# Kernel optimization log

Measured on AMD Instinct MI355X. Metric: run time of the kernel, lower is better.

## Reference

```python
import jax, jax.numpy as jnp
import numpy as np

DIM = 128
NUM_TILES = 50000
NUM_PIECES = 25000
E_TT = 600000
E_PT = 400000


def _mean_aggregate(msgs, dst, num_dst):
    # msgs: [E, dim], dst: [E] int -> [num_dst, dim]
    agg = jax.ops.segment_sum(msgs, dst, num_segments=num_dst)
    cnt = jax.ops.segment_sum(jnp.ones((dst.shape[0], 1), msgs.dtype), dst,
                              num_segments=num_dst)
    return agg / jnp.maximum(cnt, 1.0)


def _linear(x, W, b):
    # torch nn.Linear: y = x @ W.T + b, W: [out, in]
    return x @ W.T + b


def setup_inputs() -> dict:
    key = jax.random.key(0)
    ks = jax.random.split(key, 20)
    s = 1.0 / np.sqrt(DIM)
    s2 = 1.0 / np.sqrt(2 * DIM)
    inp = {
        "tile_h": jax.random.normal(ks[0], (NUM_TILES, DIM), jnp.float32),
        "piece_h": jax.random.normal(ks[1], (NUM_PIECES, DIM), jnp.float32),
        "tile_src": jax.random.randint(ks[2], (E_PT,), 0, NUM_TILES),
        "piece_dst": jax.random.randint(ks[3], (E_PT,), 0, NUM_PIECES),
        "piece_src": jax.random.randint(ks[4], (E_PT,), 0, NUM_PIECES),
        "tile_dst": jax.random.randint(ks[5], (E_PT,), 0, NUM_TILES),
        "t_src": jax.random.randint(ks[6], (E_TT,), 0, NUM_TILES),
        "t_dst": jax.random.randint(ks[7], (E_TT,), 0, NUM_TILES),
        # weights: torch Linear layout [out_features, in_features]
        "W_t2p": jax.random.uniform(ks[8], (DIM, DIM), jnp.float32, -s, s),
        "b_t2p": jax.random.uniform(ks[9], (DIM,), jnp.float32, -s, s),
        "W_pu": jax.random.uniform(ks[10], (DIM, 2 * DIM), jnp.float32, -s2, s2),
        "b_pu": jax.random.uniform(ks[11], (DIM,), jnp.float32, -s2, s2),
        "W_p2t": jax.random.uniform(ks[12], (DIM, DIM), jnp.float32, -s, s),
        "b_p2t": jax.random.uniform(ks[13], (DIM,), jnp.float32, -s, s),
        "W_tup": jax.random.uniform(ks[14], (DIM, 2 * DIM), jnp.float32, -s2, s2),
        "b_tup": jax.random.uniform(ks[15], (DIM,), jnp.float32, -s2, s2),
        "W_t2t": jax.random.uniform(ks[16], (DIM, DIM), jnp.float32, -s, s),
        "b_t2t": jax.random.uniform(ks[17], (DIM,), jnp.float32, -s, s),
        "W_tut": jax.random.uniform(ks[18], (DIM, 2 * DIM), jnp.float32, -s2, s2),
        "b_tut": jax.random.uniform(ks[19], (DIM,), jnp.float32, -s2, s2),
    }
    return inp


def reference(tile_h, piece_h, tile_src, piece_dst, piece_src, tile_dst,
              t_src, t_dst,
              W_t2p, b_t2p, W_pu, b_pu, W_p2t, b_p2t,
              W_tup, b_tup, W_t2t, b_t2t, W_tut, b_tut):
    num_tiles = tile_h.shape[0]
    num_pieces = piece_h.shape[0]

    # Stage 1: tile -> piece
    msgs = _linear(tile_h[tile_src], W_t2p, b_t2p)          # [E_pt, dim]
    agg = _mean_aggregate(msgs, piece_dst, num_pieces)
    piece_h = jax.nn.relu(_linear(jnp.concatenate([piece_h, agg], axis=1), W_pu, b_pu))

    # Stage 2: piece -> tile
    msgs = _linear(piece_h[piece_src], W_p2t, b_p2t)        # [E_pt, dim]
    agg = _mean_aggregate(msgs, tile_dst, num_tiles)
    tile_h = jax.nn.relu(_linear(jnp.concatenate([tile_h, agg], axis=1), W_tup, b_tup))

    # Stage 3: tile -> tile
    msgs = _linear(tile_h[t_src], W_t2t, b_t2t)             # [E_tt, dim]
    agg = _mean_aggregate(msgs, t_dst, num_tiles)
    tile_h = jax.nn.relu(_linear(jnp.concatenate([tile_h, agg], axis=1), W_tut, b_tut))

    return (tile_h, piece_h)
```

## Files before the change

kernel.cpp:

```cpp
#include <hip/hip_runtime.h>
#include <hip/hip_bf16.h>

#define DIM 128
#define EPB 4096
#define BINS 512

typedef unsigned short u16;
typedef unsigned int u32;
typedef __attribute__((ext_vector_type(8))) short v8s;
typedef __attribute__((ext_vector_type(4))) float v4f;

__device__ __forceinline__ float bf2f(u16 u) {
    union { unsigned int i; float f; } v;
    v.i = ((unsigned int)u) << 16;
    return v.f;
}

__device__ __forceinline__ u16 f2bf(float f) {
    union { float f; unsigned int i; } v;
    v.f = f;
    unsigned int x = v.i;
    return (u16)((x + 0x7fffu + ((x >> 16) & 1u)) >> 16);
}

__device__ __forceinline__ uint4 pack8(float4 x0, float4 x1) {
    uint4 o;
    o.x = (u32)f2bf(x0.x) | ((u32)f2bf(x0.y) << 16);
    o.y = (u32)f2bf(x0.z) | ((u32)f2bf(x0.w) << 16);
    o.z = (u32)f2bf(x1.x) | ((u32)f2bf(x1.y) << 16);
    o.w = (u32)f2bf(x1.z) | ((u32)f2bf(x1.w) << 16);
    return o;
}

struct CvtArgs { const float* s[8]; u32 pfx[9]; };
__global__ __launch_bounds__(256) void cvt_and_count(
    CvtArgs a, u16* __restrict__ dst, int n8, int cvtB,
    const int* __restrict__ piece_dst, const int* __restrict__ tile_dst,
    const int* __restrict__ t_dst, int EPT, int ETT,
    int* __restrict__ counts, int NBLK)
{
    __shared__ int h[BINS];
    const int t = threadIdx.x;
    if (blockIdx.x < cvtB) {
        int g = blockIdx.x * 256 + t;
        if (g >= n8) return;
        u32 flat = (u32)g * 8;
        int seg = 0;
        #pragma unroll
        for (int i = 1; i < 8; ++i) if (flat >= a.pfx[i]) seg = i;
        const float4* fp = (const float4*)(a.s[seg] + (flat - a.pfx[seg]));
        *(uint4*)(dst + flat) = pack8(fp[0], fp[1]);
        return;
    }
    const int blk = blockIdx.x - cvtB;
    for (int d = t; d < BINS; d += 256) h[d] = 0;
    __syncthreads();
    const int ET = 2 * EPT + ETT;
    #pragma unroll 4
    for (int j = 0; j < EPB / 256; ++j) {
        int e = blk * EPB + j * 256 + t;
        if (e < ET) {
            int d;
            if (e < EPT)            d = (piece_dst[e] >> 9);
            else if (e < 2 * EPT)   d = 128 | (tile_dst[e - EPT] >> 9);
            else                    d = 256 | (t_dst[e - 2 * EPT] >> 9);
            atomicAdd(&h[d], 1);
        }
    }
    __syncthreads();
    for (int d = t; d < BINS; d += 256) counts[d * NBLK + blk] = h[d];
}

__global__ __launch_bounds__(256) void scan_gpart(const int* __restrict__ in,
                                                  int* __restrict__ out,
                                                  int* __restrict__ bsum, int n)
{
    __shared__ int ls[256];
    const int blk = blockIdx.x, t = threadIdx.x;
    const int base = blk * 2048;
    int v[8]; int s = 0;
    #pragma unroll
    for (int i = 0; i < 8; ++i) {
        int idx = base + t * 8 + i;
        v[i] = (idx < n) ? in[idx] : 0;
        s += v[i];
    }
    ls[t] = s;
    __syncthreads();
    #pragma unroll
    for (int o = 1; o < 256; o <<= 1) {
        int x = (t >= o) ? ls[t - o] : 0;
        __syncthreads();
        ls[t] += x;
        __syncthreads();
    }
    int run = (t == 0) ? 0 : ls[t - 1];
    #pragma unroll
    for (int i = 0; i < 8; ++i) {
        int idx = base + t * 8 + i;
        if (idx < n) out[idx] = run;
        run += v[i];
    }
    if (t == 255) bsum[blk] = ls[255];
}

__global__ __launch_bounds__(512) void rs_scatter(
    const int* __restrict__ tile_src, const int* __restrict__ piece_dst,
    const int* __restrict__ piece_src, const int* __restrict__ tile_dst,
    const int* __restrict__ t_src, const int* __restrict__ t_dst,
    int EPT, int ETT,
    const int* __restrict__ countsS, const int* __restrict__ bsum, int SB,
    int NBLK, int* __restrict__ T)
{
    __shared__ int p[BINS];
    __shared__ int offp[128];
    const int t = threadIdx.x;
    const int blk = blockIdx.x;
    if (t < SB) offp[t] = bsum[t];
    __syncthreads();
    if (t == 0) {
        int run = 0;
        for (int i = 0; i < SB; ++i) { int v = offp[i]; offp[i] = run; run += v; }
    }
    __syncthreads();
    if (t < BINS) {
        int idx = t * NBLK + blk;
        p[t] = countsS[idx] + offp[idx >> 11];
    }
    __syncthreads();
    const int ET = 2 * EPT + ETT;
    #pragma unroll 4
    for (int j = 0; j < EPB / 512; ++j) {
        int e = blk * EPB + j * 512 + t;
        if (e < ET) {
            int dst, src, d;
            if (e < EPT) {
                dst = piece_dst[e]; src = tile_src[e]; d = dst >> 9;
            } else if (e < 2 * EPT) {
                int le = e - EPT;
                dst = tile_dst[le]; src = piece_src[le]; d = 128 | (dst >> 9);
            } else {
                int le = e - 2 * EPT;
                dst = t_dst[le]; src = t_src[le]; d = 256 | (dst >> 9);
            }
            int pos = atomicAdd(&p[d], 1);
            T[pos] = ((dst & 511) << 17) | src;
        }
    }
}

__global__ __launch_bounds__(512) void bucket_sort(
    const int* __restrict__ T, const int* __restrict__ countsS,
    const int* __restrict__ bsum, int SB, int NBLK, int ET,
    int EPT, int ETT, int NP, int NT,
    int* __restrict__ el, int* __restrict__ rowptr)
{
    const int d = blockIdx.x;
    const int seg = d >> 7;
    if (seg > 2) return;
    const int dhi = d & 127;
    int Nseg, segOff, rb, Eseg;
    if (seg == 0)      { Nseg = NP; segOff = 0;       rb = 0;                 Eseg = EPT; }
    else if (seg == 1) { Nseg = NT; segOff = EPT;     rb = NP + 1;            Eseg = EPT; }
    else               { Nseg = NT; segOff = 2 * EPT; rb = NP + 1 + NT + 1;   Eseg = ETT; }

    __shared__ int hist[BINS];
    __shared__ int pos[BINS];
    __shared__ int ls[BINS];
    __shared__ int offp[128];
    const int t = threadIdx.x;
    if (t < SB) offp[t] = bsum[t];
    __syncthreads();
    if (t == 0) {
        int run = 0;
        for (int i = 0; i < SB; ++i) { int v = offp[i]; offp[i] = run; run += v; }
    }
    __syncthreads();
    int i0 = d * NBLK;
    const int bstart = countsS[i0] + offp[i0 >> 11];
    int bend;
    if (d < BINS - 1) { int i1 = (d + 1) * NBLK; bend = countsS[i1] + offp[i1 >> 11]; }
    else bend = ET;

    if (t < BINS) hist[t] = 0;
    __syncthreads();
    for (int j = bstart + t; j < bend; j += 512)
        atomicAdd(&hist[T[j] >> 17], 1);
    __syncthreads();
    int c0 = (t < BINS) ? hist[t] : 0;
    ls[t & (BINS - 1)] = 0;
    ls[t] = c0;
    __syncthreads();
    #pragma unroll
    for (int o = 1; o < BINS; o <<= 1) {
        int x = (t >= o) ? ls[t - o] : 0;
        __syncthreads();
        ls[t] += x;
        __syncthreads();
    }
    int ex = (t == 0) ? 0 : ls[t - 1];
    pos[t] = bstart + ex;
    __syncthreads();
    {
        int n = dhi * 512 + t;
        if (n < Nseg) rowptr[rb + n] = pos[t] - segOff;
    }
    if (t == 0 && dhi == ((Nseg - 1) >> 9)) rowptr[rb + Nseg] = Eseg;
    __syncthreads();
    for (int j = bstart + t; j < bend; j += 512) {
        int v = T[j];
        int p = atomicAdd(&pos[v >> 17], 1);
        el[p] = v & 0x1ffff;
    }
}

#define GACC(vv, p0, p1, p2, p3, p4, p5, p6, p7) do { \
    p0 += bf2f((u16)((vv).x & 0xffffu)); p1 += bf2f((u16)((vv).x >> 16)); \
    p2 += bf2f((u16)((vv).y & 0xffffu)); p3 += bf2f((u16)((vv).y >> 16)); \
    p4 += bf2f((u16)((vv).z & 0xffffu)); p5 += bf2f((u16)((vv).z >> 16)); \
    p6 += bf2f((u16)((vv).w & 0xffffu)); p7 += bf2f((u16)((vv).w >> 16)); } while (0)

__global__ __launch_bounds__(256) void gather_mean_kernel(
    const u16* __restrict__ feat,
    const int* __restrict__ elist, const int* __restrict__ rowptr,
    int N, u16* __restrict__ meanA)
{
    int node = blockIdx.x * 16 + (threadIdx.x >> 4);
    int lane = threadIdx.x & 15;
    if (node >= N) return;
    int r0 = rowptr[node], r1 = rowptr[node + 1];
    float a0 = 0.f, a1 = 0.f, a2 = 0.f, a3 = 0.f;
    float a4 = 0.f, a5 = 0.f, a6 = 0.f, a7 = 0.f;
    float b0 = 0.f, b1 = 0.f, b2 = 0.f, b3 = 0.f;
    float b4 = 0.f, b5 = 0.f, b6 = 0.f, b7 = 0.f;
    int j = r0;
    for (; j + 8 <= r1; j += 8) {
        int s0 = elist[j],     s1 = elist[j + 1], s2 = elist[j + 2], s3 = elist[j + 3];
        int s4 = elist[j + 4], s5 = elist[j + 5], s6 = elist[j + 6], s7 = elist[j + 7];
        uint4 v0 = ((const uint4*)(feat + (size_t)s0 * DIM))[lane];
        uint4 v1 = ((const uint4*)(feat + (size_t)s1 * DIM))[lane];
        uint4 v2 = ((const uint4*)(feat + (size_t)s2 * DIM))[lane];
        uint4 v3 = ((const uint4*)(feat + (size_t)s3 * DIM))[lane];
        uint4 v4 = ((const uint4*)(feat + (size_t)s4 * DIM))[lane];
        uint4 v5 = ((const uint4*)(feat + (size_t)s5 * DIM))[lane];
        uint4 v6 = ((const uint4*)(feat + (size_t)s6 * DIM))[lane];
        uint4 v7 = ((const uint4*)(feat + (size_t)s7 * DIM))[lane];
        GACC(v0, a0, a1, a2, a3, a4, a5, a6, a7);
        GACC(v1, b0, b1, b2, b3, b4, b5, b6, b7);
        GACC(v2, a0, a1, a2, a3, a4, a5, a6, a7);
        GACC(v3, b0, b1, b2, b3, b4, b5, b6, b7);
        GACC(v4, a0, a1, a2, a3, a4, a5, a6, a7);
        GACC(v5, b0, b1, b2, b3, b4, b5, b6, b7);
        GACC(v6, a0, a1, a2, a3, a4, a5, a6, a7);
        GACC(v7, b0, b1, b2, b3, b4, b5, b6, b7);
    }
    for (; j + 4 <= r1; j += 4) {
        int s0 = elist[j], s1 = elist[j + 1], s2 = elist[j + 2], s3 = elist[j + 3];
        uint4 v0 = ((const uint4*)(feat + (size_t)s0 * DIM))[lane];
        uint4 v1 = ((const uint4*)(feat + (size_t)s1 * DIM))[lane];
        uint4 v2 = ((const uint4*)(feat + (size_t)s2 * DIM))[lane];
        uint4 v3 = ((const uint4*)(feat + (size_t)s3 * DIM))[lane];
        GACC(v0, a0, a1, a2, a3, a4, a5, a6, a7);
        GACC(v1, b0, b1, b2, b3, b4, b5, b6, b7);
        GACC(v2, a0, a1, a2, a3, a4, a5, a6, a7);
        GACC(v3, b0, b1, b2, b3, b4, b5, b6, b7);
    }
    for (; j < r1; ++j) {
        int s = elist[j];
        uint4 v = ((const uint4*)(feat + (size_t)s * DIM))[lane];
        GACC(v, a0, a1, a2, a3, a4, a5, a6, a7);
    }
    a0 += b0; a1 += b1; a2 += b2; a3 += b3;
    a4 += b4; a5 += b5; a6 += b6; a7 += b7;
    float sc = (r1 > r0) ? (1.f / (float)(r1 - r0)) : 0.f;
    uint4 o;
    o.x = (u32)f2bf(a0 * sc) | ((u32)f2bf(a1 * sc) << 16);
    o.y = (u32)f2bf(a2 * sc) | ((u32)f2bf(a3 * sc) << 16);
    o.z = (u32)f2bf(a4 * sc) | ((u32)f2bf(a5 * sc) << 16);
    o.w = (u32)f2bf(a6 * sc) | ((u32)f2bf(a7 * sc) << 16);
    ((uint4*)(meanA + (size_t)node * DIM))[lane] = o;
}

__global__ __launch_bounds__(256) void stage_fused(
    const u16* __restrict__ meanA, const int* __restrict__ rowptr,
    const u16* __restrict__ Wt, const float* __restrict__ bt,
    const u16* __restrict__ A1, const u16* __restrict__ Wu,
    const float* __restrict__ bu,
    u16* __restrict__ outC, float* __restrict__ outF, int N)
{
    __shared__ u16 Wl[128][136];
    __shared__ u16 Al[64][136];
    const int tid = threadIdx.x;
    const int nb = blockIdx.x * 64;
    const int wave = tid >> 6;
    const int lane = tid & 63;
    const int m = lane & 15;
    const int quad = lane >> 4;
    const int arow = wave * 16 + m;

    #pragma unroll
    for (int i = 0; i < 8; ++i) {
        int c = i * 256 + tid;
        int row = c >> 4;
        int c8 = (c & 15) * 8;
        *(uint4*)&Wl[row][c8] = *(const uint4*)(Wt + row * 128 + c8);
    }
    #pragma unroll
    for (int i = 0; i < 4; ++i) {
        int c = i * 256 + tid;
        int row = c >> 4;
        int c8 = (c & 15) * 8;
        int n = nb + row;
        uint4 v = {0u, 0u, 0u, 0u};
        if (n < N) v = *(const uint4*)(meanA + (size_t)n * DIM + c8);
        *(uint4*)&Al[row][c8] = v;
    }
    __syncthreads();

    v4f acct[8];
    #pragma unroll
    for (int t = 0; t < 8; ++t) acct[t] = (v4f){0.f, 0.f, 0.f, 0.f};
    #pragma unroll
    for (int k0 = 0; k0 < 128; k0 += 32) {
        v8s a = *(const v8s*)&Al[arow][k0 + quad * 8];
        #pragma unroll
        for (int t = 0; t < 8; ++t) {
            v8s b = *(const v8s*)&Wl[t * 16 + m][k0 + quad * 8];
            acct[t] = __builtin_amdgcn_mfma_f32_16x16x32_bf16(a, b, acct[t], 0, 0, 0);
        }
    }
    __syncthreads();

    {
        float btv[8];
        #pragma unroll
        for (int t = 0; t < 8; ++t) btv[t] = bt[t * 16 + m];
        #pragma unroll
        for (int r = 0; r < 4; ++r) {
            int n = nb + wave * 16 + quad * 4 + r;
            bool has = (n < N) && (rowptr[n + 1] > rowptr[n]);
            #pragma unroll
            for (int t = 0; t < 8; ++t) {
                float val = has ? (acct[t][r] + btv[t]) : 0.f;
                Al[wave * 16 + quad * 4 + r][t * 16 + m] = f2bf(val);
            }
        }
    }
    #pragma unroll
    for (int i = 0; i < 8; ++i) {
        int c = i * 256 + tid;
        int row = c >> 4;
        int c8 = (c & 15) * 8;
        *(uint4*)&Wl[row][c8] = *(const uint4*)(Wu + row * 256 + 128 + c8);
    }
    __syncthreads();

    v4f accu[8];
    #pragma unroll
    for (int t = 0; t < 8; ++t) accu[t] = (v4f){0.f, 0.f, 0.f, 0.f};
    #pragma unroll
    for (int k0 = 0; k0 < 128; k0 += 32) {
        v8s a = *(const v8s*)&Al[arow][k0 + quad * 8];
        #pragma unroll
        for (int t = 0; t < 8; ++t) {
            v8s b = *(const v8s*)&Wl[t * 16 + m][k0 + quad * 8];
            accu[t] = __builtin_amdgcn_mfma_f32_16x16x32_bf16(a, b, accu[t], 0, 0, 0);
        }
    }
    __syncthreads();

    #pragma unroll
    for (int i = 0; i < 8; ++i) {
        int c = i * 256 + tid;
        int row = c >> 4;
        int c8 = (c & 15) * 8;
        *(uint4*)&Wl[row][c8] = *(const uint4*)(Wu + row * 256 + c8);
    }
    #pragma unroll
    for (int i = 0; i < 4; ++i) {
        int c = i * 256 + tid;
        int row = c >> 4;
        int c8 = (c & 15) * 8;
        int n = nb + row;
        uint4 v = {0u, 0u, 0u, 0u};
        if (n < N) v = *(const uint4*)(A1 + (size_t)n * DIM + c8);
        *(uint4*)&Al[row][c8] = v;
    }
    __syncthreads();

    #pragma unroll
    for (int k0 = 0; k0 < 128; k0 += 32) {
        v8s a = *(const v8s*)&Al[arow][k0 + quad * 8];
        #pragma unroll
        for (int t = 0; t < 8; ++t) {
            v8s b = *(const v8s*)&Wl[t * 16 + m][k0 + quad * 8];
            accu[t] = __builtin_amdgcn_mfma_f32_16x16x32_bf16(a, b, accu[t], 0, 0, 0);
        }
    }

    float buv[8];
    #pragma unroll
    for (int t = 0; t < 8; ++t) buv[t] = bu[t * 16 + m];
    #pragma unroll
    for (int r = 0; r < 4; ++r) {
        int n = nb + wave * 16 + quad * 4 + r;
        if (n >= N) continue;
        #pragma unroll
        for (int t = 0; t < 8; ++t) {
            float val = accu[t][r] + buv[t];
            val = val > 0.f ? val : 0.f;
            if (outC) outC[(size_t)n * DIM + t * 16 + m] = f2bf(val);
            if (outF) outF[(size_t)n * DIM + t * 16 + m] = val;
        }
    }
}

extern "C" void kernel_launch(void* const* d_in, const int* in_sizes, int n_in,
                              void* d_out, int out_size, void* d_ws, size_t ws_size,
                              hipStream_t stream)
{
    const float* tile_h   = (const float*)d_in[0];
    const float* piece_h  = (const float*)d_in[1];
    const int* tile_src   = (const int*)d_in[2];
    const int* piece_dst  = (const int*)d_in[3];
    const int* piece_src  = (const int*)d_in[4];
    const int* tile_dst   = (const int*)d_in[5];
    const int* t_src      = (const int*)d_in[6];
    const int* t_dst      = (const int*)d_in[7];
    const float* b_t2p = (const float*)d_in[9];
    const float* b_pu  = (const float*)d_in[11];
    const float* b_p2t = (const float*)d_in[13];
    const float* b_tup = (const float*)d_in[15];
    const float* b_t2t = (const float*)d_in[17];
    const float* b_tut = (const float*)d_in[19];

    const int NT  = in_sizes[0] / DIM;
    const int NP  = in_sizes[1] / DIM;
    const int EPT = in_sizes[2];
    const int ETT = in_sizes[6];
    const int ET  = 2 * EPT + ETT;

    const int NBLK = (ET + EPB - 1) / EPB;
    const int n2 = BINS * NBLK;
    const int SB = (n2 + 2047) / 2048;

    char* ws = (char*)d_ws;
    size_t off = 0;
    int* counts = (int*)(ws + off);   off += (size_t)n2 * sizeof(int);
    off = (off + 255) & ~(size_t)255;
    int* countsS = (int*)(ws + off);  off += (size_t)n2 * sizeof(int);
    off = (off + 255) & ~(size_t)255;
    int* gbsum = (int*)(ws + off);    off += (size_t)((SB + 63) & ~63) * sizeof(int);
    off = (off + 255) & ~(size_t)255;
    int* rowptr = (int*)(ws + off);   off += (size_t)(NP + 2 * NT + 3) * sizeof(int);
    off = (off + 255) & ~(size_t)255;
    int* el = (int*)(ws + off);       off += (size_t)ET * sizeof(int);
    off = (off + 255) & ~(size_t)255;
    u16* A = (u16*)(ws + off);        off += (size_t)NT * DIM * sizeof(u16);
    off = (off + 255) & ~(size_t)255;
    u16* C = (u16*)(ws + off);        off += (size_t)NT * DIM * sizeof(u16);
    off = (off + 255) & ~(size_t)255;
    u16* arena = (u16*)(ws + off);

    int* T = (int*)A;

    const u32 nTh = (u32)NT * DIM, nPh = (u32)NP * DIM;
    u32 pfx[9];
    pfx[0] = 0;
    pfx[1] = nTh;
    pfx[2] = pfx[1] + nPh;
    pfx[3] = pfx[2] + 16384;
    pfx[4] = pfx[3] + 32768;
    pfx[5] = pfx[4] + 16384;
    pfx[6] = pfx[5] + 32768;
    pfx[7] = pfx[6] + 16384;
    pfx[8] = pfx[7] + 32768;

    u16* Th = arena + pfx[0];
    u16* Ph = arena + pfx[1];
    const u16* Wt2p = arena + pfx[2];
    const u16* Wpu  = arena + pfx[3];
    const u16* Wp2t = arena + pfx[4];
    const u16* Wtup = arena + pfx[5];
    const u16* Wt2t = arena + pfx[6];
    const u16* Wtut = arena + pfx[7];

    int* rp1 = rowptr;
    int* rp2 = rowptr + NP + 1;
    int* rp3 = rowptr + NP + 1 + NT + 1;
    int* el1 = el;
    int* el2 = el + EPT;
    int* el3 = el + 2 * EPT;

    float* out_tile  = (float*)d_out;
    float* out_piece = out_tile + (size_t)NT * DIM;

    dim3 blk(256);
    dim3 blk2(512);
    int n8 = (int)(pfx[8] / 8);
    const int cvtB = (n8 + 255) / 256;
    dim3 g_fat((unsigned)(cvtB + NBLK));
    dim3 g_rs((unsigned)NBLK);
    dim3 g_scan((unsigned)SB);
    dim3 g_bs((unsigned)BINS);
    dim3 g_gp((unsigned)((NP + 15) / 16));
    dim3 g_gt((unsigned)((NT + 15) / 16));
    dim3 g_np((unsigned)((NP + 63) / 64));
    dim3 g_nt((unsigned)((NT + 63) / 64));

    CvtArgs ca;
    ca.s[0] = tile_h; ca.s[1] = piece_h;
    ca.s[2] = (const float*)d_in[8];  ca.s[3] = (const float*)d_in[10];
    ca.s[4] = (const float*)d_in[12]; ca.s[5] = (const float*)d_in[14];
    ca.s[6] = (const float*)d_in[16]; ca.s[7] = (const float*)d_in[18];
    for (int i = 0; i < 9; ++i) ca.pfx[i] = pfx[i];
    hipLaunchKernelGGL(cvt_and_count, g_fat, blk, 0, stream,
                       ca, arena, n8, cvtB,
                       piece_dst, tile_dst, t_dst, EPT, ETT, counts, NBLK);

    hipLaunchKernelGGL(scan_gpart, g_scan, blk, 0, stream, counts, countsS, gbsum, n2);
    hipLaunchKernelGGL(rs_scatter, g_rs, blk2, 0, stream,
                       tile_src, piece_dst, piece_src, tile_dst, t_src, t_dst,
                       EPT, ETT, countsS, gbsum, SB, NBLK, T);
    hipLaunchKernelGGL(bucket_sort, g_bs, blk2, 0, stream,
                       T, countsS, gbsum, SB, NBLK, ET, EPT, ETT, NP, NT, el, rowptr);

    hipLaunchKernelGGL(gather_mean_kernel, g_gp, blk, 0, stream,
                       Th, el1, rp1, NP, A);
    hipLaunchKernelGGL(stage_fused, g_np, blk, 0, stream,
                       A, rp1, Wt2p, b_t2p, Ph, Wpu, b_pu, C, out_piece, NP);

    hipLaunchKernelGGL(gather_mean_kernel, g_gt, blk, 0, stream,
                       C, el2, rp2, NT, A);
    hipLaunchKernelGGL(stage_fused, g_nt, blk, 0, stream,
                       A, rp2, Wp2t, b_p2t, Th, Wtup, b_tup, C, (float*)nullptr, NT);

    hipLaunchKernelGGL(gather_mean_kernel, g_gt, blk, 0, stream,
                       C, el3, rp3, NT, A);
    hipLaunchKernelGGL(stage_fused, g_nt, blk, 0, stream,
                       A, rp3, Wt2t, b_t2t, C, Wtut, b_tut, (u16*)nullptr, out_tile, NT);
}
```

Before: 291.1 us.

## Merge CSR build kernels into one cooperative kernel with grid syncs

Replaces the four preprocessing kernels (convert+count, scan, radix scatter, bucket sort) with a single cooperative launch of 512 blocks of 512 threads that separates the phases with grid.sync(). The weight/feature conversion now uses a grid-stride loop, and the scan covers 2048 entries per block with 4 values per thread. The aim is to remove per-kernel launch gaps and tail drain between the small CSR-building stages. The cost is the grid-wide barriers, and it depends on all 512 blocks being co-resident and on NBLK, SB and BINS fitting the fixed grid size.

```diff
diff --git a/kernel.cpp b/kernel.cpp
--- a/kernel.cpp
+++ b/kernel.cpp
@@ -1,9 +1,14 @@
 #include <hip/hip_runtime.h>
 #include <hip/hip_bf16.h>
+#include <hip/hip_cooperative_groups.h>
+
+namespace cg = cooperative_groups;
 
 #define DIM 128
 #define EPB 4096
 #define BINS 512
+#define CBLK 512
+#define CTHR 512
 
 typedef unsigned short u16;
 typedef unsigned int u32;
@@ -33,184 +38,166 @@
 }
 
 struct CvtArgs { const float* s[8]; u32 pfx[9]; };
-__global__ __launch_bounds__(256) void cvt_and_count(
-    CvtArgs a, u16* __restrict__ dst, int n8, int cvtB,
-    const int* __restrict__ piece_dst, const int* __restrict__ tile_dst,
-    const int* __restrict__ t_dst, int EPT, int ETT,
-    int* __restrict__ counts, int NBLK)
-{
-    __shared__ int h[BINS];
-    const int t = threadIdx.x;
-    if (blockIdx.x < cvtB) {
-        int g = blockIdx.x * 256 + t;
-        if (g >= n8) return;
-        u32 flat = (u32)g * 8;
-        int seg = 0;
-        #pragma unroll
-        for (int i = 1; i < 8; ++i) if (flat >= a.pfx[i]) seg = i;
-        const float4* fp = (const float4*)(a.s[seg] + (flat - a.pfx[seg]));
-        *(uint4*)(dst + flat) = pack8(fp[0], fp[1]);
-        return;
-    }
-    const int blk = blockIdx.x - cvtB;
-    for (int d = t; d < BINS; d += 256) h[d] = 0;
-    __syncthreads();
-    const int ET = 2 * EPT + ETT;
-    #pragma unroll 4
-    for (int j = 0; j < EPB / 256; ++j) {
-        int e = blk * EPB + j * 256 + t;
-        if (e < ET) {
-            int d;
-            if (e < EPT)            d = (piece_dst[e] >> 9);
-            else if (e < 2 * EPT)   d = 128 | (tile_dst[e - EPT] >> 9);
-            else                    d = 256 | (t_dst[e - 2 * EPT] >> 9);
-            atomicAdd(&h[d], 1);
-        }
-    }
-    __syncthreads();
-    for (int d = t; d < BINS; d += 256) counts[d * NBLK + blk] = h[d];
-}
-
-__global__ __launch_bounds__(256) void scan_gpart(const int* __restrict__ in,
-                                                  int* __restrict__ out,
-                                                  int* __restrict__ bsum, int n)
-{
-    __shared__ int ls[256];
-    const int blk = blockIdx.x, t = threadIdx.x;
-    const int base = blk * 2048;
-    int v[8]; int s = 0;
-    #pragma unroll
-    for (int i = 0; i < 8; ++i) {
-        int idx = base + t * 8 + i;
-        v[i] = (idx < n) ? in[idx] : 0;
-        s += v[i];
-    }
-    ls[t] = s;
-    __syncthreads();
-    #pragma unroll
-    for (int o = 1; o < 256; o <<= 1) {
-        int x = (t >= o) ? ls[t - o] : 0;
-        __syncthreads();
-        ls[t] += x;
-        __syncthreads();
-    }
-    int run = (t == 0) ? 0 : ls[t - 1];
-    #pragma unroll
-    for (int i = 0; i < 8; ++i) {
-        int idx = base + t * 8 + i;
-        if (idx < n) out[idx] = run;
-        run += v[i];
-    }
-    if (t == 255) bsum[blk] = ls[255];
-}
-
-__global__ __launch_bounds__(512) void rs_scatter(
+
+__global__ __launch_bounds__(CTHR) void csr_coop(
+    CvtArgs a, u16* __restrict__ cdst, int n8,
     const int* __restrict__ tile_src, const int* __restrict__ piece_dst,
     const int* __restrict__ piece_src, const int* __restrict__ tile_dst,
     const int* __restrict__ t_src, const int* __restrict__ t_dst,
-    int EPT, int ETT,
-    const int* __restrict__ countsS, const int* __restrict__ bsum, int SB,
-    int NBLK, int* __restrict__ T)
+    int EPT, int ETT, int NP, int NT,
+    int* __restrict__ counts, int* __restrict__ countsS,
+    int* __restrict__ bsum, int NBLK, int n2, int SB,
+    int* __restrict__ T, int* __restrict__ el, int* __restrict__ rowptr)
 {
-    __shared__ int p[BINS];
+    cg::grid_group grid = cg::this_grid();
+    __shared__ int sh[BINS];
+    __shared__ int sh2[BINS];
+    __shared__ int sh3[BINS];
     __shared__ int offp[128];
     const int t = threadIdx.x;
-    const int blk = blockIdx.x;
-    if (t < SB) offp[t] = bsum[t];
-    __syncthreads();
-    if (t == 0) {
-        int run = 0;
-        for (int i = 0; i < SB; ++i) { int v = offp[i]; offp[i] = run; run += v; }
-    }
-    __syncthreads();
-    if (t < BINS) {
-        int idx = t * NBLK + blk;
-        p[t] = countsS[idx] + offp[idx >> 11];
-    }
-    __syncthreads();
+    const int b = blockIdx.x;
     const int ET = 2 * EPT + ETT;
-    #pragma unroll 4
-    for (int j = 0; j < EPB / 512; ++j) {
-        int e = blk * EPB + j * 512 + t;
-        if (e < ET) {
-            int dst, src, d;
-            if (e < EPT) {
-                dst = piece_dst[e]; src = tile_src[e]; d = dst >> 9;
-            } else if (e < 2 * EPT) {
-                int le = e - EPT;
-                dst = tile_dst[le]; src = piece_src[le]; d = 128 | (dst >> 9);
-            } else {
-                int le = e - 2 * EPT;
-                dst = t_dst[le]; src = t_src[le]; d = 256 | (dst >> 9);
+
+    if (b < NBLK) {
+        sh[t & (BINS - 1)] = 0;
+        __syncthreads();
+        #pragma unroll
+        for (int j = 0; j < EPB / CTHR; ++j) {
+            int e = b * EPB + j * CTHR + t;
+            if (e < ET) {
+                int d;
+                if (e < EPT)            d = (piece_dst[e] >> 9);
+                else if (e < 2 * EPT)   d = 128 | (tile_dst[e - EPT] >> 9);
+                else                    d = 256 | (t_dst[e - 2 * EPT] >> 9);
+                atomicAdd(&sh[d], 1);
             }
-            int pos = atomicAdd(&p[d], 1);
-            T[pos] = ((dst & 511) << 17) | src;
-        }
-    }
-}
-
-__global__ __launch_bounds__(512) void bucket_sort(
-    const int* __restrict__ T, const int* __restrict__ countsS,
-    const int* __restrict__ bsum, int SB, int NBLK, int ET,
-    int EPT, int ETT, int NP, int NT,
-    int* __restrict__ el, int* __restrict__ rowptr)
-{
-    const int d = blockIdx.x;
-    const int seg = d >> 7;
-    if (seg > 2) return;
-    const int dhi = d & 127;
-    int Nseg, segOff, rb, Eseg;
-    if (seg == 0)      { Nseg = NP; segOff = 0;       rb = 0;                 Eseg = EPT; }
-    else if (seg == 1) { Nseg = NT; segOff = EPT;     rb = NP + 1;            Eseg = EPT; }
-    else               { Nseg = NT; segOff = 2 * EPT; rb = NP + 1 + NT + 1;   Eseg = ETT; }
-
-    __shared__ int hist[BINS];
-    __shared__ int pos[BINS];
-    __shared__ int ls[BINS];
-    __shared__ int offp[128];
-    const int t = threadIdx.x;
-    if (t < SB) offp[t] = bsum[t];
-    __syncthreads();
-    if (t == 0) {
-        int run = 0;
-        for (int i = 0; i < SB; ++i) { int v = offp[i]; offp[i] = run; run += v; }
-    }
-    __syncthreads();
-    int i0 = d * NBLK;
-    const int bstart = countsS[i0] + offp[i0 >> 11];
-    int bend;
-    if (d < BINS - 1) { int i1 = (d + 1) * NBLK; bend = countsS[i1] + offp[i1 >> 11]; }
-    else bend = ET;
-
-    if (t < BINS) hist[t] = 0;
-    __syncthreads();
-    for (int j = bstart + t; j < bend; j += 512)
-        atomicAdd(&hist[T[j] >> 17], 1);
-    __syncthreads();
-    int c0 = (t < BINS) ? hist[t] : 0;
-    ls[t & (BINS - 1)] = 0;
-    ls[t] = c0;
-    __syncthreads();
-    #pragma unroll
-    for (int o = 1; o < BINS; o <<= 1) {
-        int x = (t >= o) ? ls[t - o] : 0;
-        __syncthreads();
-        ls[t] += x;
-        __syncthreads();
-    }
-    int ex = (t == 0) ? 0 : ls[t - 1];
-    pos[t] = bstart + ex;
-    __syncthreads();
+        }
+        __syncthreads();
+        counts[t * NBLK + b] = sh[t];
+    }
+    for (int g = b * CTHR + t; g < n8; g += CBLK * CTHR) {
+        u32 flat = (u32)g * 8;
+        int seg = 0;
+        #pragma unroll
+        for (int i = 1; i < 8; ++i) if (flat >= a.pfx[i]) seg = i;
+        const float4* fp = (const float4*)(a.s[seg] + (flat - a.pfx[seg]));
+        *(uint4*)(cdst + flat) = pack8(fp[0], fp[1]);
+    }
+    grid.sync();
+
+    if (b < SB) {
+        const int base = b * 2048;
+        int v[4]; int s = 0;
+        #pragma unroll
+        for (int i = 0; i < 4; ++i) {
+            int idx = base + t * 4 + i;
+            v[i] = (idx < n2) ? counts[idx] : 0;
+            s += v[i];
+        }
+        sh[t] = s;
+        __syncthreads();
+        for (int o = 1; o < CTHR; o <<= 1) {
+            int x = (t >= o) ? sh[t - o] : 0;
+            __syncthreads();
+            sh[t] += x;
+            __syncthreads();
+        }
+        int run = (t == 0) ? 0 : sh[t - 1];
+        #pragma unroll
+        for (int i = 0; i < 4; ++i) {
+            int idx = base + t * 4 + i;
+            if (idx < n2) countsS[idx] = run;
+            run += v[i];
+        }
+        if (t == CTHR - 1) bsum[b] = sh[CTHR - 1];
+    }
+    grid.sync();
+
+    if (b < NBLK) {
+        if (t < SB) offp[t] = bsum[t];
+        __syncthreads();
+        if (t == 0) {
+            int run = 0;
+            for (int i = 0; i < SB; ++i) { int v = offp[i]; offp[i] = run; run += v; }
+        }
+        __syncthreads();
+        {
+            int idx = t * NBLK + b;
+            sh[t] = countsS[idx] + offp[idx >> 11];
+        }
+        __syncthreads();
+        #pragma unroll
+        for (int j = 0; j < EPB / CTHR; ++j) {
+            int e = b * EPB + j * CTHR + t;
+            if (e < ET) {
+                int dst, src, d;
+                if (e < EPT) {
+                    dst = piece_dst[e]; src = tile_src[e]; d = dst >> 9;
+                } else if (e < 2 * EPT) {
+                    int le = e - EPT;
+                    dst = tile_dst[le]; src = piece_src[le]; d = 128 | (dst >> 9);
+                } else {
+                    int le = e - 2 * EPT;
+                    dst = t_dst[le]; src = t_src[le]; d = 256 | (dst >> 9);
+                }
+                int pos = atomicAdd(&sh[d], 1);
+                T[pos] = ((dst & 511) << 17) | src;
+            }
+        }
+    }
+    grid.sync();
+
     {
-        int n = dhi * 512 + t;
-        if (n < Nseg) rowptr[rb + n] = pos[t] - segOff;
-    }
-    if (t == 0 && dhi == ((Nseg - 1) >> 9)) rowptr[rb + Nseg] = Eseg;
-    __syncthreads();
-    for (int j = bstart + t; j < bend; j += 512) {
-        int v = T[j];
-        int p = atomicAdd(&pos[v >> 17], 1);
-        el[p] = v & 0x1ffff;
+        const int d = b;
+        const int seg = d >> 7;
+        const int dhi = d & 127;
+        int Nseg, segOff, rb, Eseg;
+        if (seg == 0)      { Nseg = NP; segOff = 0;       rb = 0;                 Eseg = EPT; }
+        else if (seg == 1) { Nseg = NT; segOff = EPT;     rb = NP + 1;            Eseg = EPT; }
+        else               { Nseg = NT; segOff = 2 * EPT; rb = NP + 1 + NT + 1;   Eseg = ETT; }
+
+        if (t < SB) offp[t] = bsum[t];
+        __syncthreads();
+        if (t == 0) {
+            int run = 0;
+            for (int i = 0; i < SB; ++i) { int v = offp[i]; offp[i] = run; run += v; }
+        }
+        __syncthreads();
+        int i0 = d * NBLK;
+        const int bstart = countsS[i0] + offp[i0 >> 11];
+        int bend;
+        if (d < BINS - 1) { int i1 = (d + 1) * NBLK; bend = countsS[i1] + offp[i1 >> 11]; }
+        else bend = ET;
+
+        sh[t] = 0;
+        __syncthreads();
+        for (int j = bstart + t; j < bend; j += CTHR)
+            atomicAdd(&sh[T[j] >> 17], 1);
+        __syncthreads();
+        int c0 = sh[t];
+        sh3[t] = c0;
+        __syncthreads();
+        #pragma unroll
+        for (int o = 1; o < BINS; o <<= 1) {
+            int x = (t >= o) ? sh3[t - o] : 0;
+            __syncthreads();
+            sh3[t] += x;
+            __syncthreads();
+        }
+        int ex = (t == 0) ? 0 : sh3[t - 1];
+        sh2[t] = bstart + ex;
+        __syncthreads();
+        {
+            int n = dhi * 512 + t;
+            if (n < Nseg) rowptr[rb + n] = sh2[t] - segOff;
+        }
+        if (t == 0 && dhi == ((Nseg - 1) >> 9)) rowptr[rb + Nseg] = Eseg;
+        __syncthreads();
+        for (int j = bstart + t; j < bend; j += CTHR) {
+            int v = T[j];
+            int p = atomicAdd(&sh2[v >> 17], 1);
+            el[p] = v & 0x1ffff;
+        }
     }
 }
 
@@ -496,13 +483,7 @@
     float* out_piece = out_tile + (size_t)NT * DIM;
 
     dim3 blk(256);
-    dim3 blk2(512);
     int n8 = (int)(pfx[8] / 8);
-    const int cvtB = (n8 + 255) / 256;
-    dim3 g_fat((unsigned)(cvtB + NBLK));
-    dim3 g_rs((unsigned)NBLK);
-    dim3 g_scan((unsigned)SB);
-    dim3 g_bs((unsigned)BINS);
     dim3 g_gp((unsigned)((NP + 15) / 16));
     dim3 g_gt((unsigned)((NT + 15) / 16));
     dim3 g_np((unsigned)((NP + 63) / 64));
@@ -514,16 +495,24 @@
     ca.s[4] = (const float*)d_in[12]; ca.s[5] = (const float*)d_in[14];
     ca.s[6] = (const float*)d_in[16]; ca.s[7] = (const float*)d_in[18];
     for (int i = 0; i < 9; ++i) ca.pfx[i] = pfx[i];
-    hipLaunchKernelGGL(cvt_and_count, g_fat, blk, 0, stream,
-                       ca, arena, n8, cvtB,
-                       piece_dst, tile_dst, t_dst, EPT, ETT, counts, NBLK);
-
-    hipLaunchKernelGGL(scan_gpart, g_scan, blk, 0, stream, counts, countsS, gbsum, n2);
-    hipLaunchKernelGGL(rs_scatter, g_rs, blk2, 0, stream,
-                       tile_src, piece_dst, piece_src, tile_dst, t_src, t_dst,
-                       EPT, ETT, countsS, gbsum, SB, NBLK, T);
-    hipLaunchKernelGGL(bucket_sort, g_bs, blk2, 0, stream,
-                       T, countsS, gbsum, SB, NBLK, ET, EPT, ETT, NP, NT, el, rowptr);
+
+    int n8v = n8, eptv = EPT, ettv = ETT, npv = NP, ntv = NT;
+    int nblkv = NBLK, n2v = n2, sbv = SB;
+    u16* arenav = arena;
+    const int* tsv = tile_src; const int* pdv = piece_dst;
+    const int* psv = piece_src; const int* tdv = tile_dst;
+    const int* ttsv = t_src; const int* ttdv = t_dst;
+    int* countsv = counts; int* countsSv = countsS; int* gbsumv = gbsum;
+    int* Tv = T; int* elv = el; int* rowptrv = rowptr;
+    void* cargs[] = {
+        &ca, &arenav, &n8v,
+        &tsv, &pdv, &psv, &tdv, &ttsv, &ttdv,
+        &eptv, &ettv, &npv, &ntv,
+        &countsv, &countsSv, &gbsumv, &nblkv, &n2v, &sbv,
+        &Tv, &elv, &rowptrv
+    };
+    hipLaunchCooperativeKernel((void*)csr_coop, dim3(CBLK), dim3(CTHR),
+                               cargs, 0, stream);
 
     hipLaunchKernelGGL(gather_mean_kernel, g_gp, blk, 0, stream,
                        Th, el1, rp1, NP, A);
```

After: 525.9 us. +80.7%, slower.
